# Performance work log

Measured on AMD Instinct MI355X. Metric: run time of the kernel, lower is better.

The kernel has to match this reference:

```python
import jax, jax.numpy as jnp
import numpy as np

TEMPERATURE = 0.5
NORM_EPS = 1e-12  # F.normalize clamp eps
LID_EPS = 1e-12
B, DZ, DF = 4096, 128, 2048


def _off_diag(x):
    # remove the diagonal of an [n, n] matrix -> [n, n-1], row-major order
    n = x.shape[0]
    return x.reshape(-1)[1:].reshape(n - 1, n + 1)[:, :-1].reshape(n, n - 1)


def _lid_mle(data, reference, k):
    # pairwise euclidean distances (cdist)
    d2 = (jnp.sum(data * data, axis=1, keepdims=True)
          + jnp.sum(reference * reference, axis=1)[None, :]
          - 2.0 * data @ reference.T)
    dists = jnp.sqrt(jnp.clip(d2, 0.0, None))
    # k+1 smallest (first is the zero self-distance), ascending
    neg_top, _ = jax.lax.top_k(-dists, k + 1)
    d = -neg_top[:, 1:]            # [N, k], ascending; d[:, -1] is k-th NN dist
    return -k / jnp.sum(jnp.log(d / d[:, -1:] + LID_EPS), axis=1)


def setup_inputs() -> dict:
    key = jax.random.key(0)
    k0, k1, k2, k3 = jax.random.split(key, 4)
    return {
        "z_0": jax.random.normal(k0, (B, DZ), jnp.float32),
        "z_1": jax.random.normal(k1, (B, DZ), jnp.float32),
        "f_0": jax.random.normal(k2, (B, DF), jnp.float32),
        "f_1": jax.random.normal(k3, (B, DF), jnp.float32),
    }


def reference(z_0, z_1, f_0, f_1):
    b = z_0.shape[0]
    # F.normalize(dim=1)
    z0 = z_0 / jnp.maximum(jnp.linalg.norm(z_0, axis=1, keepdims=True), NORM_EPS)
    z1 = z_1 / jnp.maximum(jnp.linalg.norm(z_1, axis=1, keepdims=True), NORM_EPS)

    logits_00 = jnp.einsum('nc,mc->nm', z0, z0) / TEMPERATURE
    logits_01 = jnp.einsum('nc,mc->nm', z0, z1) / TEMPERATURE
    logits_10 = jnp.einsum('nc,mc->nm', z1, z0) / TEMPERATURE
    logits_11 = jnp.einsum('nc,mc->nm', z1, z1) / TEMPERATURE

    logits_00 = _off_diag(logits_00)   # [b, b-1]
    logits_11 = _off_diag(logits_11)   # [b, b-1]

    logits = jnp.concatenate([
        jnp.concatenate([logits_01, logits_00], axis=1),
        jnp.concatenate([logits_10, logits_11], axis=1),
    ], axis=0)                          # [2b, 2b-1]
    logits = jnp.nan_to_num(logits, nan=0.0, posinf=0.0, neginf=0.0)

    labels = jnp.tile(jnp.arange(b, dtype=jnp.int32), 2)  # rank = 0

    logp = jax.nn.log_softmax(logits, axis=1)
    loss_per = -jnp.take_along_axis(logp, labels[:, None], axis=1)[:, 0]
    loss_per = jnp.nan_to_num(loss_per, nan=0.1, posinf=0.1, neginf=0.1)
    loss = jnp.mean(loss_per)

    # track_lid (no-grad auxiliary metric)
    f = jnp.concatenate([f_0, f_1], axis=0)
    lids_k32 = _lid_mle(f, f, 32)
    lids_k512 = _lid_mle(f, f, 512)

    return loss, logits, labels, lids_k32, lids_k512
```

## Files before the change

### kernel.cpp

```cpp
#include <hip/hip_runtime.h>
#include <math.h>

#define B_   4096
#define DZ   128
#define DF   2048
#define N2   8192
#define NL   8191

#define OFF_LOGITS 1
#define OFF_LAB  (1 + (size_t)N2 * NL)
#define OFF_L32  (OFF_LAB + N2)
#define OFF_L512 (OFF_L32 + N2)

#define WS_ZN 0
#define WS_FN ((size_t)N2 * DZ)
#define WS_LP (WS_FN + N2)
#define WS_FCOMB (WS_LP + N2)

typedef __attribute__((ext_vector_type(8))) __bf16 bf16x8;
typedef __attribute__((ext_vector_type(8))) unsigned short ushort8;
typedef __attribute__((ext_vector_type(4))) float f32x4;

__device__ __forceinline__ unsigned short f2bf(float f) {
  unsigned u = __float_as_uint(f);
  return (unsigned short)((u + 0x7FFFu + ((u >> 16) & 1u)) >> 16);
}
__device__ __forceinline__ float bf2f(unsigned short h) {
  return __uint_as_float(((unsigned)h) << 16);
}

__global__ __launch_bounds__(256) void fnorm_kernel(const float* __restrict__ f0,
                                                    const float* __restrict__ f1,
                                                    float* __restrict__ fn) {
  int r = blockIdx.x;
  const float* row = (r < B_) ? f0 + (size_t)r * DF : f1 + (size_t)(r - B_) * DF;
  float s = 0.f;
  for (int j = threadIdx.x; j < DF; j += 256) { float v = row[j]; s += v * v; }
  for (int off = 32; off; off >>= 1) s += __shfl_down(s, off, 64);
  __shared__ float red[4];
  if ((threadIdx.x & 63) == 0) red[threadIdx.x >> 6] = s;
  __syncthreads();
  if (threadIdx.x == 0) fn[r] = red[0] + red[1] + red[2] + red[3];
}

__global__ __launch_bounds__(256) void convert_kernel(const float* __restrict__ f0,
                                                      const float* __restrict__ f1,
                                                      unsigned short* __restrict__ fcomb,
                                                      float* __restrict__ fn) {
  int r = blockIdx.x, t = threadIdx.x;
  const float* row = (r < B_) ? f0 + (size_t)r * DF : f1 + (size_t)(r - B_) * DF;
  float4 v0 = *(const float4*)(row + t * 8);
  float4 v1 = *(const float4*)(row + t * 8 + 4);
  float v[8] = {v0.x, v0.y, v0.z, v0.w, v1.x, v1.y, v1.z, v1.w};
  ushort8 h, l;
  float s = 0.f;
#pragma unroll
  for (int j = 0; j < 8; j++) {
    unsigned short hb = f2bf(v[j]);
    h[j] = hb;
    l[j] = f2bf(v[j] - bf2f(hb));
    s += v[j] * v[j];
  }
  unsigned short* rowp = fcomb + (size_t)r * (2 * DF);
  int slab = t >> 2, c = t & 3;
  *(ushort8*)(rowp + slab * 64 + c * 8) = h;
  *(ushort8*)(rowp + slab * 64 + 32 + c * 8) = l;
  for (int off = 32; off; off >>= 1) s += __shfl_down(s, off, 64);
  __shared__ float red[4];
  if ((t & 63) == 0) red[t >> 6] = s;
  __syncthreads();
  if (t == 0) fn[r] = red[0] + red[1] + red[2] + red[3];
}

__global__ void znorm_kernel(const float* __restrict__ z0, const float* __restrict__ z1,
                             float* __restrict__ zn) {
  int r = blockIdx.x, t = threadIdx.x;
  const float* row = (r < B_) ? z0 + (size_t)r * DZ : z1 + (size_t)(r - B_) * DZ;
  float v = row[t];
  float s = v * v;
  for (int off = 32; off; off >>= 1) s += __shfl_down(s, off, 64);
  __shared__ float red[2];
  if ((t & 63) == 0) red[t >> 6] = s;
  __syncthreads();
  float n = sqrtf(red[0] + red[1]);
  zn[(size_t)r * DZ + t] = v / fmaxf(n, 1e-12f);
}

__global__ __launch_bounds__(256) void d2_gemm_pre_kernel(const unsigned short* __restrict__ fcomb,
                                                          const float* __restrict__ fn,
                                                          float* __restrict__ D2) {
  int bj = blockIdx.x, bi = blockIdx.y;
  if (bi > bj) return;
  const int ib = bi * 128, jb = bj * 128;

  __shared__ __attribute__((aligned(16))) unsigned short TILE[2][2 * 128 * 64];

  const int tid = threadIdx.x;
  const int lane = tid & 63;
  const int wave = tid >> 6;
  const int wr = (wave >> 1) * 64;
  const int wc = (wave & 1) * 64;
  const int m  = lane & 15;
  const int kg = lane >> 4;

  const int lrow8 = lane >> 3;
  const int lchk  = (lane & 7) ^ lrow8;
  const int grow0 = ((wave < 2) ? ib : jb) + (wave & 1) * 64;
  const char* gsrc = (const char*)fcomb + (size_t)(grow0 + lrow8) * 8192 + (size_t)lchk * 16;

  f32x4 acc[4][4];
#pragma unroll
  for (int i = 0; i < 4; i++)
#pragma unroll
    for (int j = 0; j < 4; j++) acc[i][j] = (f32x4)0.f;

  {
    char* lds0 = (char*)&TILE[0][0] + wave * 8192;
#pragma unroll
    for (int i = 0; i < 8; i++)
      __builtin_amdgcn_global_load_lds(
          (const __attribute__((address_space(1))) void*)(gsrc + (size_t)i * 65536),
          (__attribute__((address_space(3))) void*)(lds0 + i * 1024), 16, 0, 0);
    gsrc += 128;
  }
  asm volatile("s_waitcnt vmcnt(0)" ::: "memory");
  __builtin_amdgcn_s_barrier();
  __builtin_amdgcn_sched_barrier(0);

  for (int s = 0; s < 64; ++s) {
    const int cur = s & 1;
    if (s < 63) {
      char* ldsn = (char*)&TILE[cur ^ 1][0] + wave * 8192;
#pragma unroll
      for (int i = 0; i < 8; i++)
        __builtin_amdgcn_global_load_lds(
            (const __attribute__((address_space(1))) void*)(gsrc + (size_t)i * 65536),
            (__attribute__((address_space(3))) void*)(ldsn + i * 1024), 16, 0, 0);
      gsrc += 128;
    }

    const unsigned short* T = &TILE[cur][0];
    bf16x8 a_h[4], a_l[4], b_h[4], b_l[4];
#pragma unroll
    for (int t4 = 0; t4 < 4; t4++) {
      int ra = wr + t4 * 16 + m;
      int rb = wc + t4 * 16 + m;
      int sa = ra & 7, sb = rb & 7;
      a_h[t4] = *(const bf16x8*)&T[ra * 64 + ((kg ^ sa) << 3)];
      a_l[t4] = *(const bf16x8*)&T[ra * 64 + (((kg | 4) ^ sa) << 3)];
      b_h[t4] = *(const bf16x8*)&T[8192 + rb * 64 + ((kg ^ sb) << 3)];
      b_l[t4] = *(const bf16x8*)&T[8192 + rb * 64 + (((kg | 4) ^ sb) << 3)];
    }
#pragma unroll
    for (int ti = 0; ti < 4; ti++)
#pragma unroll
      for (int tj = 0; tj < 4; tj++) {
        acc[ti][tj] = __builtin_amdgcn_mfma_f32_16x16x32_bf16(a_h[ti], b_h[tj], acc[ti][tj], 0, 0, 0);
        acc[ti][tj] = __builtin_amdgcn_mfma_f32_16x16x32_bf16(a_h[ti], b_l[tj], acc[ti][tj], 0, 0, 0);
        acc[ti][tj] = __builtin_amdgcn_mfma_f32_16x16x32_bf16(a_l[ti], b_h[tj], acc[ti][tj], 0, 0, 0);
      }

    asm volatile("s_waitcnt vmcnt(0)" ::: "memory");
    __builtin_amdgcn_s_barrier();
    __builtin_amdgcn_sched_barrier(0);
  }

#pragma unroll
  for (int ti = 0; ti < 4; ti++) {
    int irow0 = ib + wr + ti * 16 + kg * 4;
    float4 fni = *(const float4*)&fn[irow0];
    float fniv[4] = {fni.x, fni.y, fni.z, fni.w};
#pragma unroll
    for (int tj = 0; tj < 4; tj++) {
      int jg = jb + wc + tj * 16 + m;
      float fnj = fn[jg];
      float val[4];
#pragma unroll
      for (int r = 0; r < 4; r++)
        val[r] = fmaxf(fniv[r] + fnj - 2.f * acc[ti][tj][r], 0.f);
#pragma unroll
      for (int r = 0; r < 4; r++)
        D2[(size_t)(irow0 + r) * N2 + jg] = val[r];
      if (bi != bj)
        *(float4*)&D2[(size_t)jg * N2 + irow0] = make_float4(val[0], val[1], val[2], val[3]);
    }
  }
}

#define LSTR 40
__global__ __launch_bounds__(256) void d2_gemm_mfma_kernel(const float* __restrict__ f0,
                                                           const float* __restrict__ f1,
                                                           const float* __restrict__ fn,
                                                           float* __restrict__ D2) {
  int bj = blockIdx.x, bi = blockIdx.y;
  if (bi > bj) return;
  const int ib = bi * 128, jb = bj * 128;
  const float* Ab = (ib < B_) ? f0 + (size_t)ib * DF : f1 + (size_t)(ib - B_) * DF;
  const float* Bb = (jb < B_) ? f0 + (size_t)jb * DF : f1 + (size_t)(jb - B_) * DF;

  __shared__ __attribute__((aligned(16))) unsigned short Ah[128 * LSTR];
  __shared__ __attribute__((aligned(16))) unsigned short Al[128 * LSTR];
  __shared__ __attribute__((aligned(16))) unsigned short Bh[128 * LSTR];
  __shared__ __attribute__((aligned(16))) unsigned short Bl[128 * LSTR];

  const int tid = threadIdx.x;
  const int lane = tid & 63;
  const int wave = tid >> 6;
  const int wr = (wave >> 1) * 64;
  const int wc = (wave & 1) * 64;
  const int m  = lane & 15;
  const int kg = lane >> 4;

  const int lrow = tid >> 1;
  const int lhalf = tid & 1;
  const float* arow = Ab + (size_t)lrow * DF + lhalf * 16;
  const float* brow = Bb + (size_t)lrow * DF + lhalf * 16;
  const int wbase = lrow * LSTR + lhalf * 16;

  f32x4 acc[4][4];
#pragma unroll
  for (int i = 0; i < 4; i++)
#pragma unroll
    for (int j = 0; j < 4; j++) acc[i][j] = (f32x4)0.f;

  for (int k0 = 0; k0 < DF; k0 += 32) {
    float av[16], bv[16];
#pragma unroll
    for (int q = 0; q < 4; q++) {
      float4 t = *(const float4*)(arow + k0 + q * 4);
      av[q * 4 + 0] = t.x; av[q * 4 + 1] = t.y; av[q * 4 + 2] = t.z; av[q * 4 + 3] = t.w;
    }
#pragma unroll
    for (int q = 0; q < 4; q++) {
      float4 t = *(const float4*)(brow + k0 + q * 4);
      bv[q * 4 + 0] = t.x; bv[q * 4 + 1] = t.y; bv[q * 4 + 2] = t.z; bv[q * 4 + 3] = t.w;
    }

    __syncthreads();

    ushort8 ah0, ah1, al0, al1, bh0, bh1, bl0, bl1;
#pragma unroll
    for (int j = 0; j < 8; j++) {
      unsigned short h = f2bf(av[j]);     ah0[j] = h; al0[j] = f2bf(av[j] - bf2f(h));
      unsigned short h2 = f2bf(av[j + 8]); ah1[j] = h2; al1[j] = f2bf(av[j + 8] - bf2f(h2));
      unsigned short h3 = f2bf(bv[j]);     bh0[j] = h3; bl0[j] = f2bf(bv[j] - bf2f(h3));
      unsigned short h4 = f2bf(bv[j + 8]); bh1[j] = h4; bl1[j] = f2bf(bv[j + 8] - bf2f(h4));
    }
    *(ushort8*)&Ah[wbase] = ah0;     *(ushort8*)&Ah[wbase + 8] = ah1;
    *(ushort8*)&Al[wbase] = al0;     *(ushort8*)&Al[wbase + 8] = al1;
    *(ushort8*)&Bh[wbase] = bh0;     *(ushort8*)&Bh[wbase + 8] = bh1;
    *(ushort8*)&Bl[wbase] = bl0;     *(ushort8*)&Bl[wbase + 8] = bl1;

    __syncthreads();

    bf16x8 a_h[4], a_l[4], b_h[4], b_l[4];
#pragma unroll
    for (int t4 = 0; t4 < 4; t4++) {
      int aoff = (wr + t4 * 16 + m) * LSTR + kg * 8;
      int boff = (wc + t4 * 16 + m) * LSTR + kg * 8;
      a_h[t4] = *(const bf16x8*)&Ah[aoff];
      a_l[t4] = *(const bf16x8*)&Al[aoff];
      b_h[t4] = *(const bf16x8*)&Bh[boff];
      b_l[t4] = *(const bf16x8*)&Bl[boff];
    }
#pragma unroll
    for (int ti = 0; ti < 4; ti++)
#pragma unroll
      for (int tj = 0; tj < 4; tj++) {
        acc[ti][tj] = __builtin_amdgcn_mfma_f32_16x16x32_bf16(a_h[ti], b_h[tj], acc[ti][tj], 0, 0, 0);
        acc[ti][tj] = __builtin_amdgcn_mfma_f32_16x16x32_bf16(a_h[ti], b_l[tj], acc[ti][tj], 0, 0, 0);
        acc[ti][tj] = __builtin_amdgcn_mfma_f32_16x16x32_bf16(a_l[ti], b_h[tj], acc[ti][tj], 0, 0, 0);
      }
  }

#pragma unroll
  for (int ti = 0; ti < 4; ti++) {
    int irow0 = ib + wr + ti * 16 + kg * 4;
    float4 fni = *(const float4*)&fn[irow0];
    float fniv[4] = {fni.x, fni.y, fni.z, fni.w};
#pragma unroll
    for (int tj = 0; tj < 4; tj++) {
      int jg = jb + wc + tj * 16 + m;
      float fnj = fn[jg];
      float val[4];
#pragma unroll
      for (int r = 0; r < 4; r++)
        val[r] = fmaxf(fniv[r] + fnj - 2.f * acc[ti][tj][r], 0.f);
#pragma unroll
      for (int r = 0; r < 4; r++)
        D2[(size_t)(irow0 + r) * N2 + jg] = val[r];
      if (bi != bj)
        *(float4*)&D2[(size_t)jg * N2 + irow0] = make_float4(val[0], val[1], val[2], val[3]);
    }
  }
}

__global__ __launch_bounds__(256) void select_lid_kernel(const float* __restrict__ D2,
                                                         float* __restrict__ out) {
  int r = blockIdx.x, tid = threadIdx.x;
  const float* row = D2 + (size_t)r * N2;
  unsigned key[32];
#pragma unroll
  for (int j = 0; j < 32; j++) {
    float v = fmaxf(row[tid + j * 256], 0.f);
    key[j] = __float_as_uint(v);
  }
  __shared__ int wcnt[32][4];
  __shared__ int pref[256];
  __shared__ unsigned cand[512];
  __shared__ float rr[8];

  unsigned T = 0;
  for (int b = 30; b >= 0; b--) {
    unsigned t = T | (1u << b);
    int c = 0;
#pragma unroll
    for (int j = 0; j < 32; j++) c += (key[j] < t) ? 1 : 0;
    for (int off = 32; off; off >>= 1) c += __shfl_down(c, off, 64);
    if ((tid & 63) == 0) wcnt[b][tid >> 6] = c;
    __syncthreads();
    int tot = wcnt[b][0] + wcnt[b][1] + wcnt[b][2] + wcnt[b][3];
    if (tot <= 512) T = t;
  }

  int n_t = 0;
#pragma unroll
  for (int j = 0; j < 32; j++) n_t += (key[j] < T) ? 1 : 0;
  pref[tid] = n_t;
  __syncthreads();
  for (int s = 1; s < 256; s <<= 1) {
    int v = (tid >= s) ? pref[tid - s] : 0;
    __syncthreads();
    pref[tid] += v;
    __syncthreads();
  }
  int c0 = pref[255];
  int base = pref[tid] - n_t;
  cand[tid] = 0xFFFFFFFFu;
  cand[tid + 256] = 0xFFFFFFFFu;
  __syncthreads();
  {
    int idx = base;
#pragma unroll
    for (int j = 0; j < 32; j++)
      if (key[j] < T) cand[idx++] = key[j];
  }
  __syncthreads();

  for (int k = 2; k <= 512; k <<= 1) {
    for (int j = k >> 1; j > 0; j >>= 1) {
      int i = ((tid & ~(j - 1)) << 1) | (tid & (j - 1));
      int p = i | j;
      bool up = (i & k) == 0;
      unsigned a = cand[i], b2 = cand[p];
      if ((a > b2) == up) { cand[i] = b2; cand[p] = a; }
      __syncthreads();
    }
  }

  float d32  = sqrtf(__uint_as_float(32  < c0 ? cand[32]  : T));
  float d512 = sqrtf(__uint_as_float(512 < c0 ? cand[512] : T));
  int i1 = tid + 1, i2 = tid + 257;
  float di1 = sqrtf(__uint_as_float(i1 < c0 ? cand[i1] : T));
  float di2 = sqrtf(__uint_as_float(i2 < c0 ? cand[i2] : T));
  float s32 = (i1 <= 32) ? logf(di1 / d32 + 1e-12f) : 0.f;
  float s512 = logf(di1 / d512 + 1e-12f) + logf(di2 / d512 + 1e-12f);
  for (int off = 32; off; off >>= 1) {
    s32 += __shfl_down(s32, off, 64);
    s512 += __shfl_down(s512, off, 64);
  }
  if ((tid & 63) == 0) { rr[tid >> 6] = s32; rr[4 + (tid >> 6)] = s512; }
  __syncthreads();
  if (tid == 0) {
    float S32 = rr[0] + rr[1] + rr[2] + rr[3];
    float S512 = rr[4] + rr[5] + rr[6] + rr[7];
    out[OFF_L32 + r] = -32.f / S32;
    out[OFF_L512 + r] = -512.f / S512;
  }
}

__global__ __launch_bounds__(256) void zgram_logits_kernel(const float* __restrict__ zn,
                                                           float* __restrict__ out) {
  int bj = blockIdx.x, bi = blockIdx.y;
  const int ib = bi * 128, jb = bj * 128;
  const float* Ab = zn + (size_t)ib * DZ;
  const float* Bb = zn + (size_t)jb * DZ;

  __shared__ __attribute__((aligned(16))) float As[16][128];
  __shared__ __attribute__((aligned(16))) float Bs[16][128];

  int tid = threadIdx.x;
  int tx = tid & 15, ty = tid >> 4;
  int lrow = tid >> 1;
  int lk = (tid & 1) * 8;

  float acc[8][8];
#pragma unroll
  for (int i = 0; i < 8; i++)
#pragma unroll
    for (int j = 0; j < 8; j++) acc[i][j] = 0.f;

  for (int k0 = 0; k0 < DZ; k0 += 16) {
    float4 a0 = *(const float4*)(Ab + (size_t)lrow * DZ + k0 + lk);
    float4 a1 = *(const float4*)(Ab + (size_t)lrow * DZ + k0 + lk + 4);
    float4 b0 = *(const float4*)(Bb + (size_t)lrow * DZ + k0 + lk);
    float4 b1 = *(const float4*)(Bb + (size_t)lrow * DZ + k0 + lk + 4);
    __syncthreads();
    As[lk + 0][lrow] = a0.x; As[lk + 1][lrow] = a0.y; As[lk + 2][lrow] = a0.z; As[lk + 3][lrow] = a0.w;
    As[lk + 4][lrow] = a1.x; As[lk + 5][lrow] = a1.y; As[lk + 6][lrow] = a1.z; As[lk + 7][lrow] = a1.w;
    Bs[lk + 0][lrow] = b0.x; Bs[lk + 1][lrow] = b0.y; Bs[lk + 2][lrow] = b0.z; Bs[lk + 3][lrow] = b0.w;
    Bs[lk + 4][lrow] = b1.x; Bs[lk + 5][lrow] = b1.y; Bs[lk + 6][lrow] = b1.z; Bs[lk + 7][lrow] = b1.w;
    __syncthreads();
#pragma unroll
    for (int kk = 0; kk < 16; kk++) {
      float4 av0 = *(const float4*)&As[kk][ty * 8];
      float4 av1 = *(const float4*)&As[kk][ty * 8 + 4];
      float4 bv0 = *(const float4*)&Bs[kk][tx * 4];
      float4 bv1 = *(const float4*)&Bs[kk][tx * 4 + 64];
      float a_[8] = {av0.x, av0.y, av0.z, av0.w, av1.x, av1.y, av1.z, av1.w};
      float b_[8] = {bv0.x, bv0.y, bv0.z, bv0.w, bv1.x, bv1.y, bv1.z, bv1.w};
#pragma unroll
      for (int v = 0; v < 8; v++)
#pragma unroll
        for (int u = 0; u < 8; u++) acc[v][u] += a_[v] * b_[u];
    }
  }

#pragma unroll
  for (int v = 0; v < 8; v++) {
    int rrow = ib + ty * 8 + v;
#pragma unroll
    for (int u = 0; u < 8; u++) {
      int c = jb + tx * 4 + (u & 3) + (u >> 2) * 64;
      if (c == rrow) continue;
      float lg = 2.f * acc[v][u];
      int col;
      if (rrow < B_) col = (c >= B_) ? (c - B_) : (B_ + c - (c > rrow ? 1 : 0));
      else           col = (c < B_) ? c : (c - (c > rrow ? 1 : 0));
      out[OFF_LOGITS + (size_t)rrow * NL + col] = lg;
    }
  }
}

__global__ void labels_kernel(float* __restrict__ out) {
  int i = blockIdx.x * 256 + threadIdx.x;
  if (i < N2) out[OFF_LAB + i] = (float)(i & (B_ - 1));
}

__global__ __launch_bounds__(256) void loss_row_kernel(const float* __restrict__ out,
                                                       float* __restrict__ lossp) {
  int r = blockIdx.x, tid = threadIdx.x;
  const float* row = out + OFF_LOGITS + (size_t)r * NL;
  __shared__ __attribute__((aligned(16))) float buf[NL];
  __shared__ float red[4];
  float m = -1e30f;
  for (int j = tid; j < NL; j += 256) { float v = row[j]; buf[j] = v; m = fmaxf(m, v); }
  for (int off = 32; off; off >>= 1) m = fmaxf(m, __shfl_down(m, off, 64));
  if ((tid & 63) == 0) red[tid >> 6] = m;
  __syncthreads();
  m = fmaxf(fmaxf(red[0], red[1]), fmaxf(red[2], red[3]));
  float s = 0.f;
  for (int j = tid; j < NL; j += 256) s += expf(buf[j] - m);
  for (int off = 32; off; off >>= 1) s += __shfl_down(s, off, 64);
  __syncthreads();
  if ((tid & 63) == 0) red[tid >> 6] = s;
  __syncthreads();
  if (tid == 0) {
    float S = red[0] + red[1] + red[2] + red[3];
    lossp[r] = m + logf(S) - buf[r & (B_ - 1)];
  }
}

__global__ void finalize_kernel(const float* __restrict__ lossp, float* __restrict__ out) {
  int tid = threadIdx.x;
  float s = 0.f;
  for (int j = tid; j < N2; j += 256) s += lossp[j];
  for (int off = 32; off; off >>= 1) s += __shfl_down(s, off, 64);
  __shared__ float red[4];
  if ((tid & 63) == 0) red[tid >> 6] = s;
  __syncthreads();
  if (tid == 0) out[0] = (red[0] + red[1] + red[2] + red[3]) / (float)N2;
}

extern "C" void kernel_launch(void* const* d_in, const int* in_sizes, int n_in,
                              void* d_out, int out_size, void* d_ws, size_t ws_size,
                              hipStream_t stream) {
  const float* z0 = (const float*)d_in[0];
  const float* z1 = (const float*)d_in[1];
  const float* f0 = (const float*)d_in[2];
  const float* f1 = (const float*)d_in[3];
  float* out = (float*)d_out;
  float* ws = (float*)d_ws;
  float* zn = ws + WS_ZN;
  float* fn = ws + WS_FN;
  float* lp = ws + WS_LP;
  float* D2 = out;

  const size_t need_bytes = ((size_t)WS_FCOMB + (size_t)N2 * DF) * sizeof(float);
  dim3 g(64, 64);

  if (ws_size >= need_bytes) {
    unsigned short* fcomb = (unsigned short*)(ws + WS_FCOMB);
    convert_kernel<<<N2, 256, 0, stream>>>(f0, f1, fcomb, fn);
    znorm_kernel<<<N2, 128, 0, stream>>>(z0, z1, zn);
    d2_gemm_pre_kernel<<<g, 256, 0, stream>>>(fcomb, fn, D2);
  } else {
    fnorm_kernel<<<N2, 256, 0, stream>>>(f0, f1, fn);
    znorm_kernel<<<N2, 128, 0, stream>>>(z0, z1, zn);
    d2_gemm_mfma_kernel<<<g, 256, 0, stream>>>(f0, f1, fn, D2);
  }

  select_lid_kernel<<<N2, 256, 0, stream>>>(D2, out);
  zgram_logits_kernel<<<g, 256, 0, stream>>>(zn, out);
  labels_kernel<<<(N2 + 255) / 256, 256, 0, stream>>>(out);
  loss_row_kernel<<<N2, 256, 0, stream>>>(out, lp);
  finalize_kernel<<<1, 256, 0, stream>>>(lp, out);
}
```

Measured before the change: 1.248 ms.

## Compute z-gram logits with split-bf16 MFMA using pre-packed hi/lo operands

Adds a normalization kernel that writes the normalized z rows as interleaved bf16 high/low halves in a swizzled layout. A new MFMA Gram kernel streams these through LDS with async global-to-LDS loads and double buffering, using three bf16 products per tile to approximate fp32 accuracy. It writes logits straight into the off-diagonal concatenated layout, replacing the previous zgram_logits_kernel on the workspace-rich path. The cost is a larger workspace requirement and bf16x3 precision in place of the old path's precision.

After: 1.128 ms. 1.11x faster.

```diff
diff --git a/kernel.cpp b/kernel.cpp
--- a/kernel.cpp
+++ b/kernel.cpp
@@ -16,6 +16,7 @@
 #define WS_FN ((size_t)N2 * DZ)
 #define WS_LP (WS_FN + N2)
 #define WS_FCOMB (WS_LP + N2)
+#define WS_ZCOMB (WS_FCOMB + (size_t)N2 * DF)
 
 typedef __attribute__((ext_vector_type(8))) __bf16 bf16x8;
 typedef __attribute__((ext_vector_type(8))) unsigned short ushort8;
@@ -86,6 +87,26 @@
   zn[(size_t)r * DZ + t] = v / fmaxf(n, 1e-12f);
 }
 
+__global__ void znorm2_kernel(const float* __restrict__ z0, const float* __restrict__ z1,
+                              unsigned short* __restrict__ zcomb) {
+  int r = blockIdx.x, t = threadIdx.x;
+  const float* row = (r < B_) ? z0 + (size_t)r * DZ : z1 + (size_t)(r - B_) * DZ;
+  float v = row[t];
+  float s = v * v;
+  for (int off = 32; off; off >>= 1) s += __shfl_down(s, off, 64);
+  __shared__ float red[2];
+  if ((t & 63) == 0) red[t >> 6] = s;
+  __syncthreads();
+  float n = sqrtf(red[0] + red[1]);
+  float vn = v / fmaxf(n, 1e-12f);
+  unsigned short hb = f2bf(vn);
+  unsigned short lb = f2bf(vn - bf2f(hb));
+  unsigned short* rowp = zcomb + (size_t)r * 256;
+  int slab = t >> 5, p = t & 31;
+  rowp[slab * 64 + p] = hb;
+  rowp[slab * 64 + 32 + p] = lb;
+}
+
 __global__ __launch_bounds__(256) void d2_gemm_pre_kernel(const unsigned short* __restrict__ fcomb,
                                                           const float* __restrict__ fn,
                                                           float* __restrict__ D2) {
@@ -183,6 +204,103 @@
         D2[(size_t)(irow0 + r) * N2 + jg] = val[r];
       if (bi != bj)
         *(float4*)&D2[(size_t)jg * N2 + irow0] = make_float4(val[0], val[1], val[2], val[3]);
+    }
+  }
+}
+
+__global__ __launch_bounds__(256) void zgram_mfma_kernel(const unsigned short* __restrict__ zcomb,
+                                                         float* __restrict__ out) {
+  int bj = blockIdx.x, bi = blockIdx.y;
+  const int ib = bi * 128, jb = bj * 128;
+
+  __shared__ __attribute__((aligned(16))) unsigned short TILE[2][2 * 128 * 64];
+
+  const int tid = threadIdx.x;
+  const int lane = tid & 63;
+  const int wave = tid >> 6;
+  const int wr = (wave >> 1) * 64;
+  const int wc = (wave & 1) * 64;
+  const int m  = lane & 15;
+  const int kg = lane >> 4;
+
+  const int lrow8 = lane >> 3;
+  const int lchk  = (lane & 7) ^ lrow8;
+  const int grow0 = ((wave < 2) ? ib : jb) + (wave & 1) * 64;
+  const char* gsrc = (const char*)zcomb + (size_t)(grow0 + lrow8) * 512 + (size_t)lchk * 16;
+
+  f32x4 acc[4][4];
+#pragma unroll
+  for (int i = 0; i < 4; i++)
+#pragma unroll
+    for (int j = 0; j < 4; j++) acc[i][j] = (f32x4)0.f;
+
+  {
+    char* lds0 = (char*)&TILE[0][0] + wave * 8192;
+#pragma unroll
+    for (int i = 0; i < 8; i++)
+      __builtin_amdgcn_global_load_lds(
+          (const __attribute__((address_space(1))) void*)(gsrc + (size_t)i * 4096),
+          (__attribute__((address_space(3))) void*)(lds0 + i * 1024), 16, 0, 0);
+    gsrc += 128;
+  }
+  asm volatile("s_waitcnt vmcnt(0)" ::: "memory");
+  __builtin_amdgcn_s_barrier();
+  __builtin_amdgcn_sched_barrier(0);
+
+  for (int s = 0; s < 4; ++s) {
+    const int cur = s & 1;
+    if (s < 3) {
+      char* ldsn = (char*)&TILE[cur ^ 1][0] + wave * 8192;
+#pragma unroll
+      for (int i = 0; i < 8; i++)
+        __builtin_amdgcn_global_load_lds(
+            (const __attribute__((address_space(1))) void*)(gsrc + (size_t)i * 4096),
+            (__attribute__((address_space(3))) void*)(ldsn + i * 1024), 16, 0, 0);
+      gsrc += 128;
+    }
+
+    const unsigned short* T = &TILE[cur][0];
+    bf16x8 a_h[4], a_l[4], b_h[4], b_l[4];
+#pragma unroll
+    for (int t4 = 0; t4 < 4; t4++) {
+      int ra = wr + t4 * 16 + m;
+      int rb = wc + t4 * 16 + m;
+      int sa = ra & 7, sb = rb & 7;
+      a_h[t4] = *(const bf16x8*)&T[ra * 64 + ((kg ^ sa) << 3)];
+      a_l[t4] = *(const bf16x8*)&T[ra * 64 + (((kg | 4) ^ sa) << 3)];
+      b_h[t4] = *(const bf16x8*)&T[8192 + rb * 64 + ((kg ^ sb) << 3)];
+      b_l[t4] = *(const bf16x8*)&T[8192 + rb * 64 + (((kg | 4) ^ sb) << 3)];
+    }
+#pragma unroll
+    for (int ti = 0; ti < 4; ti++)
+#pragma unroll
+      for (int tj = 0; tj < 4; tj++) {
+        acc[ti][tj] = __builtin_amdgcn_mfma_f32_16x16x32_bf16(a_h[ti], b_h[tj], acc[ti][tj], 0, 0, 0);
+        acc[ti][tj] = __builtin_amdgcn_mfma_f32_16x16x32_bf16(a_h[ti], b_l[tj], acc[ti][tj], 0, 0, 0);
+        acc[ti][tj] = __builtin_amdgcn_mfma_f32_16x16x32_bf16(a_l[ti], b_h[tj], acc[ti][tj], 0, 0, 0);
+      }
+
+    asm volatile("s_waitcnt vmcnt(0)" ::: "memory");
+    __builtin_amdgcn_s_barrier();
+    __builtin_amdgcn_sched_barrier(0);
+  }
+
+#pragma unroll
+  for (int ti = 0; ti < 4; ti++) {
+    int R0 = ib + wr + ti * 16 + kg * 4;
+#pragma unroll
+    for (int tj = 0; tj < 4; tj++) {
+      int C = jb + wc + tj * 16 + m;
+#pragma unroll
+      for (int r = 0; r < 4; r++) {
+        int R = R0 + r;
+        if (C == R) continue;
+        float lg = 2.f * acc[ti][tj][r];
+        int col;
+        if (R < B_) col = (C >= B_) ? (C - B_) : (B_ + C - (C > R ? 1 : 0));
+        else        col = (C < B_) ? C : (C - (C > R ? 1 : 0));
+        out[OFF_LOGITS + (size_t)R * NL + col] = lg;
+      }
     }
   }
 }
@@ -496,22 +614,25 @@
   float* lp = ws + WS_LP;
   float* D2 = out;
 
-  const size_t need_bytes = ((size_t)WS_FCOMB + (size_t)N2 * DF) * sizeof(float);
+  const size_t need_bytes = ((size_t)WS_ZCOMB + (size_t)N2 * 128) * sizeof(float);
   dim3 g(64, 64);
 
   if (ws_size >= need_bytes) {
     unsigned short* fcomb = (unsigned short*)(ws + WS_FCOMB);
+    unsigned short* zcomb = (unsigned short*)(ws + WS_ZCOMB);
     convert_kernel<<<N2, 256, 0, stream>>>(f0, f1, fcomb, fn);
-    znorm_kernel<<<N2, 128, 0, stream>>>(z0, z1, zn);
+    znorm2_kernel<<<N2, 128, 0, stream>>>(z0, z1, zcomb);
     d2_gemm_pre_kernel<<<g, 256, 0, stream>>>(fcomb, fn, D2);
+    select_lid_kernel<<<N2, 256, 0, stream>>>(D2, out);
+    zgram_mfma_kernel<<<g, 256, 0, stream>>>(zcomb, out);
   } else {
     fnorm_kernel<<<N2, 256, 0, stream>>>(f0, f1, fn);
     znorm_kernel<<<N2, 128, 0, stream>>>(z0, z1, zn);
     d2_gemm_mfma_kernel<<<g, 256, 0, stream>>>(f0, f1, fn, D2);
-  }
-
-  select_lid_kernel<<<N2, 256, 0, stream>>>(D2, out);
-  zgram_logits_kernel<<<g, 256, 0, stream>>>(zn, out);
+    select_lid_kernel<<<N2, 256, 0, stream>>>(D2, out);
+    zgram_logits_kernel<<<g, 256, 0, stream>>>(zn, out);
+  }
+
   labels_kernel<<<(N2 + 255) / 256, 256, 0, stream>>>(out);
   loss_row_kernel<<<N2, 256, 0, stream>>>(out, lp);
   finalize_kernel<<<1, 256, 0, stream>>>(lp, out);
```
